# Kernel tuning notes

Hardware: AMD Instinct MI355X
Metric: run time of the kernel (lower is better)

Reference implementation:

```python
import jax, jax.numpy as jnp
import numpy as np
import math

B, S, H, NH = 2, 2048, 1024, 16
HD = H // NH


def setup_inputs() -> dict:
    key = jax.random.key(0)
    k1, k2, k3 = jax.random.split(key, 3)
    hidden_states = jax.random.normal(k1, (B, S, H), dtype=jnp.float32)
    attention_mask = jnp.zeros((B, 1, 1, S), dtype=jnp.float32)
    w_qkv = jax.random.normal(k2, (3 * H, H), dtype=jnp.float32) * (1.0 / math.sqrt(H))
    w_out = jax.random.normal(k3, (H, H), dtype=jnp.float32) * (1.0 / math.sqrt(H))
    gate = jnp.ones((NH,), dtype=jnp.float32)
    return {"hidden_states": hidden_states, "attention_mask": attention_mask,
            "w_qkv": w_qkv, "w_out": w_out, "gate": gate}


def reference(hidden_states, attention_mask, w_qkv, w_out, gate):
    b, s, h = hidden_states.shape
    nh, hd = NH, HD
    # fused QKV projection (no bias)
    qkv = hidden_states @ w_qkv.T                      # [b, s, 3h]
    qkv = qkv.reshape(b, s, 3, nh, hd)
    q, k, v = jnp.moveaxis(qkv, 2, 0)                  # each [b, s, nh, hd]
    q = q.transpose(0, 2, 1, 3)                        # [b, nh, s, hd]
    k = k.transpose(0, 2, 1, 3)
    v = v.transpose(0, 2, 1, 3)
    scores = jnp.einsum('bhqd,bhkd->bhqk', q, k) / math.sqrt(hd)
    scores = scores + attention_mask                   # broadcast [b,1,1,s]
    probs = jax.nn.softmax(scores, axis=-1)            # dropout p=0 -> identity
    ctx = jnp.einsum('bhqk,bhkd->bhqd', probs, v)      # [b, nh, s, hd]
    ctx = ctx.transpose(0, 2, 1, 3)                    # [b, s, nh, hd]
    ctx = ctx * gate[None, None, :, None]              # per-head gating
    ctx = ctx.reshape(b, s, h)
    out = ctx @ w_out.T
    # all gates active (> 1e-4) -> active_gates/num_heads == 1, no rescale
    return out
```

## Files before the change

### kernel.cpp

```cpp
#include <hip/hip_runtime.h>
#include <stdint.h>


typedef __attribute__((ext_vector_type(8))) short short8;
typedef __attribute__((ext_vector_type(4))) short short4v;
typedef __attribute__((ext_vector_type(4))) float floatx4;
typedef __attribute__((ext_vector_type(2))) unsigned int uint2v;

__device__ __forceinline__ unsigned short f2bf(float f) {
    unsigned int u = __float_as_uint(f);
    unsigned int r = u + 0x7fffu + ((u >> 16) & 1u);
    return (unsigned short)(r >> 16);
}
#if __has_builtin(__builtin_amdgcn_cvt_pk_bf16_f32)
__device__ __forceinline__ unsigned int pack_bf2(float lo, float hi) {
    auto v = __builtin_amdgcn_cvt_pk_bf16_f32(lo, hi);
    return __builtin_bit_cast(unsigned int, v);
}
#else
__device__ __forceinline__ unsigned int pack_bf2(float lo, float hi) {
    unsigned int a = __float_as_uint(lo) + 0x8000u;
    unsigned int b = __float_as_uint(hi) + 0x8000u;
    return __builtin_amdgcn_perm(b, a, 0x07060302u);
}
#endif

__device__ __forceinline__ void gl2lds16(const void* g, void* l) {
    __builtin_amdgcn_global_load_lds(
        (const __attribute__((address_space(1))) unsigned int*)g,
        (__attribute__((address_space(3))) unsigned int*)l, 16, 0, 0);
}

#if __has_builtin(__builtin_amdgcn_mfma_f32_16x16x16bf16_1k)
__device__ __forceinline__ void mfma16(floatx4& acc, short4v a, short4v b) {
    acc = __builtin_amdgcn_mfma_f32_16x16x16bf16_1k(a, b, acc, 0, 0, 0);
}
#elif __has_builtin(__builtin_amdgcn_mfma_f32_16x16x16_bf16)
__device__ __forceinline__ void mfma16(floatx4& acc, short4v a, short4v b) {
    acc = __builtin_amdgcn_mfma_f32_16x16x16_bf16(a, b, acc, 0, 0, 0);
}
#else
__device__ __forceinline__ void mfma16(floatx4& acc, short4v a, short4v b) {
    asm volatile("v_mfma_f32_16x16x16_bf16 %0, %1, %2, %0"
                 : "+v"(acc) : "v"(a), "v"(b));
}
#endif

__global__ __launch_bounds__(256)
void cvt_all(const float* __restrict__ a, const float* __restrict__ b,
             const float* __restrict__ c, const float* __restrict__ mask,
             unsigned short* __restrict__ oa, unsigned short* __restrict__ ob,
             unsigned short* __restrict__ oc, float* __restrict__ m2b)
{
    int i = blockIdx.x * 256 + threadIdx.x;
    if (i >= 2097152) {
        int off = i - 2097152;
        float4 v = *(const float4*)(mask + (size_t)off * 4);
        const float L2E = 1.44269504f, C2 = -14.4269504f;
        float4 w;
        w.x = fmaf(v.x, L2E, C2); w.y = fmaf(v.y, L2E, C2);
        w.z = fmaf(v.z, L2E, C2); w.w = fmaf(v.w, L2E, C2);
        *(float4*)(m2b + (size_t)off * 4) = w;
        return;
    }
    const float* src; unsigned short* dst; int off;
    if (i < 1048576)      { src = a; dst = oa; off = i; }
    else if (i < 1835008) { src = b; dst = ob; off = i - 1048576; }
    else                  { src = c; dst = oc; off = i - 1835008; }
    float4 v = *(const float4*)(src + (size_t)off * 4);
    uint2v w;
    w[0] = pack_bf2(v.x, v.y);
    w[1] = pack_bf2(v.z, v.w);
    *(uint2v*)(dst + (size_t)off * 4) = w;
}

template<int MODE, int BN>
__global__ __launch_bounds__(256)
void gemm_nt(const unsigned short* __restrict__ A,
             const unsigned short* __restrict__ Bm,
             unsigned short* __restrict__ out0,
             unsigned short* __restrict__ out1,
             unsigned short* __restrict__ out2,
             float* __restrict__ outf,
             int N)
{
    __shared__ unsigned char smem[16384 + BN * 128];
    const int K = 1024;
    const int BSL = BN / 32;
    const int tid  = threadIdx.x;
    const int wave = tid >> 6, lane = tid & 63;
    const int l15  = lane & 15, quad = lane >> 4;
    const int wm = wave >> 1, wn = wave & 1;

    int Lid = blockIdx.y * gridDim.x + blockIdx.x;
    int bm = (Lid & 7) * 4 + ((Lid >> 3) & 3);
    int bn = Lid >> 5;

    floatx4 acc[4][BSL];
#pragma unroll
    for (int i = 0; i < 4; i++)
#pragma unroll
        for (int j = 0; j < BSL; j++)
            acc[i][j] = floatx4{0.f, 0.f, 0.f, 0.f};

    int soffA[4], soffB[BSL];
#pragma unroll
    for (int l = 0; l < 4; l++) {
        int s = (wave * 4 + l) * 64 + lane;
        int row = s >> 3;
        soffA[l] = row * K + (((s & 7) ^ (row & 7)) * 8);
    }
#pragma unroll
    for (int l = 0; l < BSL; l++) {
        int s = (wave * BSL + l) * 64 + lane;
        int row = s >> 3;
        soffB[l] = row * K + (((s & 7) ^ (row & 7)) * 8);
    }

    const unsigned short* Abase = A  + (size_t)(bm * 128) * K;
    const unsigned short* Bbase = Bm + (size_t)(bn * BN) * K;

    for (int k0 = 0; k0 < K; k0 += 64) {
        __syncthreads();
#pragma unroll
        for (int l = 0; l < 4; l++)
            gl2lds16(Abase + (size_t)soffA[l] + k0, &smem[(wave * 4 + l) * 1024]);
#pragma unroll
        for (int l = 0; l < BSL; l++)
            gl2lds16(Bbase + (size_t)soffB[l] + k0, &smem[16384 + (wave * BSL + l) * 1024]);
        __syncthreads();
#pragma unroll
        for (int s2 = 0; s2 < 2; s2++) {
            short8 af[4], bfr[BSL];
            int c = s2 * 4 + quad;
#pragma unroll
            for (int i = 0; i < 4; i++) {
                int row = wm * 64 + i * 16 + l15;
                af[i] = *(const short8*)(&smem[row * 128 + ((c ^ (row & 7)) * 16)]);
            }
#pragma unroll
            for (int j = 0; j < BSL; j++) {
                int row = wn * (BN / 2) + j * 16 + l15;
                bfr[j] = *(const short8*)(&smem[16384 + row * 128 + ((c ^ (row & 7)) * 16)]);
            }
#pragma unroll
            for (int i = 0; i < 4; i++)
#pragma unroll
                for (int j = 0; j < BSL; j++)
                    acc[i][j] = __builtin_amdgcn_mfma_f32_16x16x32_bf16(af[i], bfr[j], acc[i][j], 0, 0, 0);
        }
    }

#pragma unroll
    for (int i = 0; i < 4; i++) {
#pragma unroll
        for (int j = 0; j < BSL; j++) {
            int n = bn * BN + wn * (BN / 2) + j * 16 + l15;
#pragma unroll
            for (int r = 0; r < 4; r++) {
                int m = bm * 128 + wm * 64 + i * 16 + quad * 4 + r;
                float fv = acc[i][j][r];
                if (MODE == 1) {
                    outf[(size_t)m * N + n] = fv;
                } else {
                    int t = n >> 10;
                    int h = (n >> 6) & 15;
                    int d = n & 63;
                    int b = m >> 11, si = m & 2047;
                    if (t == 2) {
                        out2[(((size_t)(b * 16 + h)) * 64 + d) * 2048 + si] = f2bf(fv);
                    } else {
                        size_t off = (((size_t)(b * 16 + h)) * 2048 + si) * 64 + d;
                        unsigned short* dst = (t == 0) ? out0 : out1;
                        dst[off] = f2bf(fv);
                    }
                }
            }
        }
    }
}

__global__ __launch_bounds__(256, 3)
void attn_kernel(const unsigned short* __restrict__ Qb,
                 const unsigned short* __restrict__ Kb,
                 const unsigned short* __restrict__ VbT,
                 const float* __restrict__ m2b,
                 const float* __restrict__ gateb,
                 unsigned short* __restrict__ ctx)
{
    __shared__ unsigned char smem[32768];
    const int S = 2048;
    const int tid  = threadIdx.x;
    const int wave = tid >> 6, lane = tid & 63;
    const int l15  = lane & 15, quad = lane >> 4;

    int Lid = blockIdx.y * gridDim.x + blockIdx.x;
    int bh = (Lid & 7) * 4 + ((Lid >> 3) & 3);
    int qc = Lid >> 5;
    const int b = bh >> 4, h = bh & 15;
    const int q0 = qc * 64 + wave * 16;

    const size_t headoff = (size_t)bh * S * 64;
    const unsigned short* Qh  = Qb  + headoff;
    const unsigned short* Kh  = Kb  + headoff;
    const unsigned short* VhT = VbT + headoff;
    const float* m2p = m2b + (size_t)b * S;

    const unsigned char* qkb[2];
#pragma unroll
    for (int s2 = 0; s2 < 2; s2++)
        qkb[s2] = &smem[l15 * 128 + (((s2 * 4 + quad) ^ (l15 & 7)) * 16)];
    const unsigned char* pvb[8];
#pragma unroll
    for (int kt = 0; kt < 8; kt++)
        pvb[kt] = &smem[16384 + l15 * 256 +
                        ((((quad >> 1) ^ (l15 & 1)) | ((kt * 2) ^ (l15 & 14))) * 16) +
                        (quad & 1) * 8];

    short8 aq[2];
#pragma unroll
    for (int s2 = 0; s2 < 2; s2++)
        aq[s2] = *(const short8*)(Qh + (size_t)(q0 + l15) * 64 + s2 * 32 + quad * 8);

    floatx4 o[4];
#pragma unroll
    for (int dt = 0; dt < 4; dt++) o[dt] = floatx4{0.f, 0.f, 0.f, 0.f};
    float l_run = 0.f;

    int koff[4], voff[4];
#pragma unroll
    for (int i = 0; i < 4; i++) {
        int s = wave * 256 + i * 64 + lane;
        int kr = s >> 3;
        koff[i] = kr * 64 + (((s & 7) ^ (kr & 7)) * 8);
        int vr = s >> 4;
        voff[i] = vr * 2048 + (((s & 15) ^ (vr & 15)) * 8);
    }

    const float C1 = 0.18033688f;

    for (int kc = 0; kc < 16; kc++) {
        const int kbase = kc * 128;
        __syncthreads();
#pragma unroll
        for (int i = 0; i < 4; i++) {
            gl2lds16(Kh + (size_t)kbase * 64 + koff[i], &smem[(wave * 4 + i) * 1024]);
            gl2lds16(VhT + (size_t)kbase + voff[i], &smem[16384 + (wave * 4 + i) * 1024]);
        }
        float4 mf[8];
#pragma unroll
        for (int t = 0; t < 8; t++)
            mf[t] = *(const float4*)(m2p + kbase + t * 16 + quad * 4);
        __syncthreads();

        floatx4 st[8];
#pragma unroll
        for (int t = 0; t < 8; t++) st[t] = floatx4{0.f, 0.f, 0.f, 0.f};
#pragma unroll
        for (int s2 = 0; s2 < 2; s2++)
#pragma unroll
            for (int t = 0; t < 8; t++) {
                short8 kf = *(const short8*)(qkb[s2] + t * 2048);
                st[t] = __builtin_amdgcn_mfma_f32_16x16x32_bf16(kf, aq[s2], st[t], 0, 0, 0);
            }

        unsigned int pw[8][2];
#pragma unroll
        for (int t = 0; t < 8; t++) {
            float e0 = exp2f(fmaf(st[t][0], C1, mf[t].x));
            float e1 = exp2f(fmaf(st[t][1], C1, mf[t].y));
            float e2 = exp2f(fmaf(st[t][2], C1, mf[t].z));
            float e3 = exp2f(fmaf(st[t][3], C1, mf[t].w));
            l_run += (e0 + e1) + (e2 + e3);
            pw[t][0] = pack_bf2(e0, e1);
            pw[t][1] = pack_bf2(e2, e3);
        }

#pragma unroll
        for (int kt = 0; kt < 8; kt++) {
            uint2v pu = {pw[kt][0], pw[kt][1]};
            short4v pb = __builtin_bit_cast(short4v, pu);
#pragma unroll
            for (int dt = 0; dt < 4; dt++) {
                uint2v vu = *(const uint2v*)(pvb[kt] + dt * 4096);
                short4v va = __builtin_bit_cast(short4v, vu);
                mfma16(o[dt], va, pb);
            }
        }
    }

    l_run += __shfl_xor(l_run, 16);
    l_run += __shfl_xor(l_run, 32);

    float gate_f = gateb[h];
    float iv = gate_f / l_run;
    size_t base = ((size_t)(b * 2048 + q0 + l15)) * 1024 + h * 64 + quad * 4;
#pragma unroll
    for (int dt = 0; dt < 4; dt++) {
        uint2v w;
        w[0] = pack_bf2(o[dt][0] * iv, o[dt][1] * iv);
        w[1] = pack_bf2(o[dt][2] * iv, o[dt][3] * iv);
        *(uint2v*)(ctx + base + dt * 16) = w;
    }
}

extern "C" void kernel_launch(void* const* d_in, const int* in_sizes, int n_in,
                              void* d_out, int out_size, void* d_ws, size_t ws_size,
                              hipStream_t stream)
{
    const float* hidden = (const float*)d_in[0];
    const float* mask   = (const float*)d_in[1];
    const float* w_qkv  = (const float*)d_in[2];
    const float* w_out  = (const float*)d_in[3];
    const float* gate   = (const float*)d_in[4];
    float* out = (float*)d_out;

    unsigned short* q_buf = (unsigned short*)d_ws;
    unsigned short* k_buf = q_buf + 4194304;
    unsigned short* v_buf = k_buf + 4194304;
    unsigned short* c_buf = v_buf + 4194304;
    unsigned short* h_bf  = c_buf + 4194304;
    unsigned short* wq_bf = h_bf  + 4194304;
    unsigned short* wo_bf = wq_bf + 3145728;
    float* m2_buf = (float*)(wo_bf + 1048576);

    cvt_all<<<8196, 256, 0, stream>>>(hidden, w_qkv, w_out, mask,
                                      h_bf, wq_bf, wo_bf, m2_buf);

    gemm_nt<0, 128><<<dim3(24, 32), 256, 0, stream>>>(h_bf, wq_bf, q_buf, k_buf, v_buf, nullptr, 3072);
    attn_kernel<<<dim3(32, 32), 256, 0, stream>>>(q_buf, k_buf, v_buf, m2_buf, gate, c_buf);
    gemm_nt<1, 64><<<dim3(16, 32), 256, 0, stream>>>(c_buf, wo_bf, nullptr, nullptr, nullptr, out, 1024);
}
```

Measured before the change: 214.0 us.

## Split attention keys across waves with per-wave double-buffered async loads

The attention kernel changes from giving each wave its own 16 query rows to having every wave handle all 64 query rows over a disjoint quarter of the key range. Each wave streams its own 32-key K/V tiles into a private double-buffered LDS region, so the block-wide barriers in the main loop go away. The row sum is now computed with an MFMA against a ones vector, and the partial outputs are combined across waves through LDS at the end. The V layout written by the QKV GEMM is permuted so that one 16-byte LDS read feeds two MFMAs. In exchange, LDS use doubles to 64 KB and more accumulator registers are needed, which lowers occupancy, and a cross-wave reduction step is added.

```diff
diff --git a/kernel.cpp b/kernel.cpp
--- a/kernel.cpp
+++ b/kernel.cpp
@@ -5,6 +5,7 @@
 typedef __attribute__((ext_vector_type(8))) short short8;
 typedef __attribute__((ext_vector_type(4))) short short4v;
 typedef __attribute__((ext_vector_type(4))) float floatx4;
+typedef __attribute__((ext_vector_type(4))) unsigned int uint4v;
 typedef __attribute__((ext_vector_type(2))) unsigned int uint2v;
 
 __device__ __forceinline__ unsigned short f2bf(float f) {
@@ -168,7 +169,9 @@
                     int d = n & 63;
                     int b = m >> 11, si = m & 2047;
                     if (t == 2) {
-                        out2[(((size_t)(b * 16 + h)) * 64 + d) * 2048 + si] = f2bf(fv);
+                        int sip = (si & ~31) | (((si >> 2) & 3) << 3)
+                                | (((si >> 4) & 1) << 2) | (si & 3);
+                        out2[(((size_t)(b * 16 + h)) * 64 + d) * 2048 + sip] = f2bf(fv);
                     } else {
                         size_t off = (((size_t)(b * 16 + h)) * 2048 + si) * 64 + d;
                         unsigned short* dst = (t == 0) ? out0 : out1;
@@ -180,7 +183,7 @@
     }
 }
 
-__global__ __launch_bounds__(256, 3)
+__global__ __launch_bounds__(256, 2)
 void attn_kernel(const unsigned short* __restrict__ Qb,
                  const unsigned short* __restrict__ Kb,
                  const unsigned short* __restrict__ VbT,
@@ -188,7 +191,7 @@
                  const float* __restrict__ gateb,
                  unsigned short* __restrict__ ctx)
 {
-    __shared__ unsigned char smem[32768];
+    __shared__ unsigned char smem[65536];
     const int S = 2048;
     const int tid  = threadIdx.x;
     const int wave = tid >> 6, lane = tid & 63;
@@ -198,7 +201,7 @@
     int bh = (Lid & 7) * 4 + ((Lid >> 3) & 3);
     int qc = Lid >> 5;
     const int b = bh >> 4, h = bh & 15;
-    const int q0 = qc * 64 + wave * 16;
+    const int q0 = qc * 64;
 
     const size_t headoff = (size_t)bh * S * 64;
     const unsigned short* Qh  = Qb  + headoff;
@@ -206,100 +209,150 @@
     const unsigned short* VhT = VbT + headoff;
     const float* m2p = m2b + (size_t)b * S;
 
-    const unsigned char* qkb[2];
+    const int WB = wave * 16384;
+
+    short8 aq[4][2];
+#pragma unroll
+    for (int sub = 0; sub < 4; sub++)
+#pragma unroll
+        for (int s2 = 0; s2 < 2; s2++)
+            aq[sub][s2] = *(const short8*)(Qh + (size_t)(q0 + sub * 16 + l15) * 64 + s2 * 32 + quad * 8);
+
+    floatx4 o[4][4];
+    floatx4 lq[4];
+#pragma unroll
+    for (int sub = 0; sub < 4; sub++) {
+        lq[sub] = floatx4{0.f, 0.f, 0.f, 0.f};
+#pragma unroll
+        for (int dt = 0; dt < 4; dt++) o[sub][dt] = floatx4{0.f, 0.f, 0.f, 0.f};
+    }
+
+    int koff[4], voff[4];
+#pragma unroll
+    for (int l = 0; l < 4; l++) {
+        int s = l * 64 + lane;
+        int key = s >> 3;
+        koff[l] = key * 64 + (((s & 7) ^ (key & 7)) * 8);
+        int d = s >> 2;
+        voff[l] = d * 2048 + (((s & 3) ^ (d & 3)) * 8);
+    }
+    int qkoff[2];
 #pragma unroll
     for (int s2 = 0; s2 < 2; s2++)
-        qkb[s2] = &smem[l15 * 128 + (((s2 * 4 + quad) ^ (l15 & 7)) * 16)];
-    const unsigned char* pvb[8];
-#pragma unroll
-    for (int kt = 0; kt < 8; kt++)
-        pvb[kt] = &smem[16384 + l15 * 256 +
-                        ((((quad >> 1) ^ (l15 & 1)) | ((kt * 2) ^ (l15 & 14))) * 16) +
-                        (quad & 1) * 8];
-
-    short8 aq[2];
-#pragma unroll
-    for (int s2 = 0; s2 < 2; s2++)
-        aq[s2] = *(const short8*)(Qh + (size_t)(q0 + l15) * 64 + s2 * 32 + quad * 8);
-
-    floatx4 o[4];
-#pragma unroll
-    for (int dt = 0; dt < 4; dt++) o[dt] = floatx4{0.f, 0.f, 0.f, 0.f};
-    float l_run = 0.f;
-
-    int koff[4], voff[4];
-#pragma unroll
-    for (int i = 0; i < 4; i++) {
-        int s = wave * 256 + i * 64 + lane;
-        int kr = s >> 3;
-        koff[i] = kr * 64 + (((s & 7) ^ (kr & 7)) * 8);
-        int vr = s >> 4;
-        voff[i] = vr * 2048 + (((s & 15) ^ (vr & 15)) * 8);
-    }
+        qkoff[s2] = l15 * 128 + (((s2 * 4 + quad) ^ (l15 & 7)) * 16);
+    const int pvoff = 4096 + l15 * 64 + ((quad ^ (l15 & 3)) * 16);
 
     const float C1 = 0.18033688f;
-
-    for (int kc = 0; kc < 16; kc++) {
-        const int kbase = kc * 128;
+    const uint2v onesu = {0x3F803F80u, 0x3F803F80u};
+    const short4v ones = __builtin_bit_cast(short4v, onesu);
+
+    {
+        const unsigned short* kg = Kh + (size_t)(wave * 32) * 64;
+        const unsigned short* vg = VhT + wave * 32;
+#pragma unroll
+        for (int l = 0; l < 4; l++) {
+            gl2lds16(kg + koff[l], &smem[WB + l * 1024]);
+            gl2lds16(vg + voff[l], &smem[WB + 4096 + l * 1024]);
+        }
+    }
+
+    for (int i = 0; i < 16; i++) {
+        const int kb = (wave + 4 * i) * 32;
+        float4 mf[2];
+#pragma unroll
+        for (int t = 0; t < 2; t++)
+            mf[t] = *(const float4*)(m2p + kb + t * 16 + quad * 4);
+        asm volatile("" ::: "memory");
+        {
+            const int kbn = (wave + 4 * ((i + 1) & 15)) * 32;
+            const int hb = WB + ((i + 1) & 1) * 8192;
+            const unsigned short* kg = Kh + (size_t)kbn * 64;
+            const unsigned short* vg = VhT + kbn;
+#pragma unroll
+            for (int l = 0; l < 4; l++) {
+                gl2lds16(kg + koff[l], &smem[hb + l * 1024]);
+                gl2lds16(vg + voff[l], &smem[hb + 4096 + l * 1024]);
+            }
+        }
+        asm volatile("s_waitcnt vmcnt(8)" ::: "memory");
+
+        const int cb = WB + (i & 1) * 8192;
+        uint4v vfu[4];
+#pragma unroll
+        for (int dt = 0; dt < 4; dt++)
+            vfu[dt] = *(const uint4v*)(&smem[cb + pvoff + dt * 1024]);
+        short8 kf[2][2];
+#pragma unroll
+        for (int t = 0; t < 2; t++)
+#pragma unroll
+            for (int s2 = 0; s2 < 2; s2++)
+                kf[t][s2] = *(const short8*)(&smem[cb + qkoff[s2] + t * 2048]);
+
+#pragma unroll
+        for (int sub = 0; sub < 4; sub++) {
+            floatx4 st[2] = {floatx4{0.f,0.f,0.f,0.f}, floatx4{0.f,0.f,0.f,0.f}};
+#pragma unroll
+            for (int s2 = 0; s2 < 2; s2++)
+#pragma unroll
+                for (int t = 0; t < 2; t++)
+                    st[t] = __builtin_amdgcn_mfma_f32_16x16x32_bf16(kf[t][s2], aq[sub][s2], st[t], 0, 0, 0);
+#pragma unroll
+            for (int t = 0; t < 2; t++) {
+                float e0 = exp2f(fmaf(st[t][0], C1, mf[t].x));
+                float e1 = exp2f(fmaf(st[t][1], C1, mf[t].y));
+                float e2 = exp2f(fmaf(st[t][2], C1, mf[t].z));
+                float e3 = exp2f(fmaf(st[t][3], C1, mf[t].w));
+                uint2v pu = {pack_bf2(e0, e1), pack_bf2(e2, e3)};
+                short4v pb = __builtin_bit_cast(short4v, pu);
+#pragma unroll
+                for (int dt = 0; dt < 4; dt++) {
+                    uint2v vh = {vfu[dt][t * 2], vfu[dt][t * 2 + 1]};
+                    short4v va = __builtin_bit_cast(short4v, vh);
+                    mfma16(o[sub][dt], va, pb);
+                }
+                mfma16(lq[sub], ones, pb);
+            }
+        }
+    }
+
+    asm volatile("s_waitcnt vmcnt(0)" ::: "memory");
+
+    floatx4 ro[4];
+#pragma unroll
+    for (int ph = 0; ph < 2; ph++) {
         __syncthreads();
 #pragma unroll
-        for (int i = 0; i < 4; i++) {
-            gl2lds16(Kh + (size_t)kbase * 64 + koff[i], &smem[(wave * 4 + i) * 1024]);
-            gl2lds16(VhT + (size_t)kbase + voff[i], &smem[16384 + (wave * 4 + i) * 1024]);
-        }
-        float4 mf[8];
-#pragma unroll
-        for (int t = 0; t < 8; t++)
-            mf[t] = *(const float4*)(m2p + kbase + t * 16 + quad * 4);
+        for (int sub = 0; sub < 4; sub++)
+#pragma unroll
+            for (int d2 = 0; d2 < 2; d2++)
+                *(floatx4*)(&smem[(((wave * 4 + sub) * 2 + d2) * 64 + lane) * 16]) = o[sub][ph * 2 + d2];
         __syncthreads();
-
-        floatx4 st[8];
-#pragma unroll
-        for (int t = 0; t < 8; t++) st[t] = floatx4{0.f, 0.f, 0.f, 0.f};
-#pragma unroll
-        for (int s2 = 0; s2 < 2; s2++)
-#pragma unroll
-            for (int t = 0; t < 8; t++) {
-                short8 kf = *(const short8*)(qkb[s2] + t * 2048);
-                st[t] = __builtin_amdgcn_mfma_f32_16x16x32_bf16(kf, aq[s2], st[t], 0, 0, 0);
-            }
-
-        unsigned int pw[8][2];
-#pragma unroll
-        for (int t = 0; t < 8; t++) {
-            float e0 = exp2f(fmaf(st[t][0], C1, mf[t].x));
-            float e1 = exp2f(fmaf(st[t][1], C1, mf[t].y));
-            float e2 = exp2f(fmaf(st[t][2], C1, mf[t].z));
-            float e3 = exp2f(fmaf(st[t][3], C1, mf[t].w));
-            l_run += (e0 + e1) + (e2 + e3);
-            pw[t][0] = pack_bf2(e0, e1);
-            pw[t][1] = pack_bf2(e2, e3);
-        }
-
-#pragma unroll
-        for (int kt = 0; kt < 8; kt++) {
-            uint2v pu = {pw[kt][0], pw[kt][1]};
-            short4v pb = __builtin_bit_cast(short4v, pu);
-#pragma unroll
-            for (int dt = 0; dt < 4; dt++) {
-                uint2v vu = *(const uint2v*)(pvb[kt] + dt * 4096);
-                short4v va = __builtin_bit_cast(short4v, vu);
-                mfma16(o[dt], va, pb);
-            }
-        }
-    }
-
-    l_run += __shfl_xor(l_run, 16);
-    l_run += __shfl_xor(l_run, 32);
-
-    float gate_f = gateb[h];
-    float iv = gate_f / l_run;
-    size_t base = ((size_t)(b * 2048 + q0 + l15)) * 1024 + h * 64 + quad * 4;
+#pragma unroll
+        for (int d2 = 0; d2 < 2; d2++) {
+            floatx4 acc = floatx4{0.f, 0.f, 0.f, 0.f};
+#pragma unroll
+            for (int w2 = 0; w2 < 4; w2++)
+                acc += *(const floatx4*)(&smem[(((w2 * 4 + wave) * 2 + d2) * 64 + lane) * 16]);
+            ro[ph * 2 + d2] = acc;
+        }
+    }
+    __syncthreads();
+#pragma unroll
+    for (int sub = 0; sub < 4; sub++)
+        *(floatx4*)(&smem[((wave * 4 + sub) * 64 + lane) * 16]) = lq[sub];
+    __syncthreads();
+    floatx4 rl = floatx4{0.f, 0.f, 0.f, 0.f};
+#pragma unroll
+    for (int w2 = 0; w2 < 4; w2++)
+        rl += *(const floatx4*)(&smem[((w2 * 4 + wave) * 64 + lane) * 16]);
+
+    float iv = gateb[h] / rl[0];
+    size_t base = ((size_t)(b * 2048 + q0 + wave * 16 + l15)) * 1024 + h * 64 + quad * 4;
 #pragma unroll
     for (int dt = 0; dt < 4; dt++) {
         uint2v w;
-        w[0] = pack_bf2(o[dt][0] * iv, o[dt][1] * iv);
-        w[1] = pack_bf2(o[dt][2] * iv, o[dt][3] * iv);
+        w[0] = pack_bf2(ro[dt][0] * iv, ro[dt][1] * iv);
+        w[1] = pack_bf2(ro[dt][2] * iv, ro[dt][3] * iv);
         *(uint2v*)(ctx + base + dt * 16) = w;
     }
 }
```

After: 209.4 us. -2.1%, faster.
